# Optimization experiments

Measured on AMD Instinct MI355X. Metric: run time of the kernel, lower is better.

The kernel has to match this reference:

```python
import jax, jax.numpy as jnp
import numpy as np

B, T, N, F, H, HEADS = 4, 10, 2048, 64, 128, 4
D = H // HEADS
E = 65536
NTOT = B * N


def setup_inputs() -> dict:
    key = jax.random.key(0)
    ks = jax.random.split(key, 16)
    s = 0.05
    return {
        "x": jax.random.normal(ks[0], (B, T, N, F), jnp.float32),
        "W": jax.random.normal(ks[1], (F, H), jnp.float32) * s,
        "att_src": jax.random.normal(ks[2], (HEADS, D), jnp.float32) * s,
        "att_dst": jax.random.normal(ks[3], (HEADS, D), jnp.float32) * s,
        "gat_bias": jnp.zeros((H,), jnp.float32),
        "W_ih0": jax.random.normal(ks[4], (4 * H, H), jnp.float32) * s,
        "W_hh0": jax.random.normal(ks[5], (4 * H, H), jnp.float32) * s,
        "b_ih0": jnp.zeros((4 * H,), jnp.float32),
        "b_hh0": jnp.zeros((4 * H,), jnp.float32),
        "W_ih1": jax.random.normal(ks[6], (4 * H, H), jnp.float32) * s,
        "W_hh1": jax.random.normal(ks[7], (4 * H, H), jnp.float32) * s,
        "b_ih1": jnp.zeros((4 * H,), jnp.float32),
        "b_hh1": jnp.zeros((4 * H,), jnp.float32),
        "ln_gamma": jnp.ones((H,), jnp.float32),
        "ln_beta": jnp.zeros((H,), jnp.float32),
        "edge_index": jax.random.randint(ks[8], (2, E), 0, NTOT, dtype=jnp.int32),
    }


def reference(x, W, att_src, att_dst, gat_bias,
              W_ih0, W_hh0, b_ih0, b_hh0,
              W_ih1, W_hh1, b_ih1, b_hh1,
              ln_gamma, ln_beta, edge_index):
    # ---- GAT spatial encoding, vectorized over all T timesteps ----
    loops = jnp.arange(NTOT, dtype=edge_index.dtype)  # PyG GATConv adds self-loops
    src = jnp.concatenate([edge_index[0], loops])
    dst = jnp.concatenate([edge_index[1], loops])

    x_flat = x.transpose(1, 0, 2, 3).reshape(T, NTOT, F)          # [T, B*N, F]
    h = (x_flat @ W).reshape(T, NTOT, HEADS, D)                    # per-head projections
    a_src = jnp.einsum('tnhd,hd->tnh', h, att_src)                 # [T, NTOT, HEADS]
    a_dst = jnp.einsum('tnhd,hd->tnh', h, att_dst)
    e = jax.nn.leaky_relu(a_src[:, src] + a_dst[:, dst], 0.2)      # [T, Ef, HEADS]

    def seg_softmax(e_t):
        m = jax.ops.segment_max(e_t, dst, num_segments=NTOT)
        ex = jnp.exp(e_t - m[dst])
        den = jax.ops.segment_sum(ex, dst, num_segments=NTOT)
        return ex / den[dst]

    alpha = jax.vmap(seg_softmax)(e)                               # edge softmax per target
    msg = alpha[..., None] * h[:, src]                             # [T, Ef, HEADS, D]
    agg = jax.vmap(lambda m: jax.ops.segment_sum(m, dst, num_segments=NTOT))(msg)
    spatial = jax.nn.relu(agg.reshape(T, NTOT, H) + gat_bias)      # concat heads + bias + relu

    # ---- 2-layer LSTM over time (batched over all B*N node sequences) ----
    def step(carry, xt):
        h0, c0, h1, c1 = carry
        g0 = xt @ W_ih0.T + h0 @ W_hh0.T + (b_ih0 + b_hh0)
        i, f, g, o = jnp.split(g0, 4, axis=-1)
        c0 = jax.nn.sigmoid(f) * c0 + jax.nn.sigmoid(i) * jnp.tanh(g)
        h0 = jax.nn.sigmoid(o) * jnp.tanh(c0)
        g1 = h0 @ W_ih1.T + h1 @ W_hh1.T + (b_ih1 + b_hh1)
        i, f, g, o = jnp.split(g1, 4, axis=-1)
        c1 = jax.nn.sigmoid(f) * c1 + jax.nn.sigmoid(i) * jnp.tanh(g)
        h1 = jax.nn.sigmoid(o) * jnp.tanh(c1)
        return (h0, c0, h1, c1), None

    z = jnp.zeros((NTOT, H), spatial.dtype)
    (_, _, h1, _), _ = jax.lax.scan(step, (z, z, z, z), spatial)
    ctx = h1.reshape(B, N, H)

    # ---- LayerNorm ----
    mu = ctx.mean(-1, keepdims=True)
    var = ctx.var(-1, keepdims=True)
    return (ctx - mu) / jnp.sqrt(var + 1e-5) * ln_gamma + ln_beta
```

## Files before the change

### kernel.cpp

```cpp
#include <hip/hip_runtime.h>

#define T_ 10
#define B_ 4
#define N_ 2048
#define NTOT 8192
#define F_ 64
#define H_ 128
#define NHEADS 4
#define D_ 32
#define E_ 65536
#define EF 73728
#define HPAD 136

typedef __bf16 bf16x8 __attribute__((ext_vector_type(8)));
typedef float f32x4 __attribute__((ext_vector_type(4)));
typedef unsigned short u16;

__device__ __forceinline__ float bf2f(u16 u){
  union { unsigned int i; float f; } v; v.i = ((unsigned int)u) << 16; return v.f;
}
__device__ __forceinline__ u16 f2bf(float f){
  union { float f; unsigned int i; } v; v.f = f;
  return (u16)((v.i + 0x7FFFu + ((v.i >> 16) & 1u)) >> 16);
}
__device__ __forceinline__ float rcpf(float x){ return __builtin_amdgcn_rcpf(x); }
__device__ __forceinline__ float sigf(float x){ return rcpf(1.f + __expf(-x)); }
__device__ __forceinline__ float tanhfast(float x){ return 1.f - 2.f * rcpf(__expf(2.f * x) + 1.f); }
__device__ __forceinline__ float lrelu(float x){ return x > 0.f ? x : 0.2f * x; }

__global__ __launch_bounds__(256) void k_init(int* __restrict__ cnt){
  int i = blockIdx.x * 256 + threadIdx.x;
  if(i < NTOT) cnt[i] = 0;
}

__global__ __launch_bounds__(256) void k_count(const int* __restrict__ ei, int* __restrict__ cnt){
  int e = blockIdx.x * 256 + threadIdx.x;
  if(e < E_) atomicAdd(&cnt[ei[E_ + e]], 1);
}

__global__ __launch_bounds__(1024) void k_scan(const int* __restrict__ cnt,
                                               int* __restrict__ rowst,
                                               int* __restrict__ cursor){
  __shared__ int lds[1024];
  const int t = threadIdx.x;
  int loc[8];
  int s = 0;
  #pragma unroll
  for(int i = 0; i < 8; i++){ loc[i] = s; s += cnt[t * 8 + i]; }
  lds[t] = s;
  __syncthreads();
  for(int off = 1; off < 1024; off <<= 1){
    int v = lds[t];
    int a = (t >= off) ? lds[t - off] : 0;
    __syncthreads();
    lds[t] = v + a;
    __syncthreads();
  }
  const int base = (t > 0) ? lds[t - 1] : 0;
  #pragma unroll
  for(int i = 0; i < 8; i++){
    rowst[t * 8 + i] = base + loc[i];
    cursor[t * 8 + i] = 0;
  }
  if(t == 1023) rowst[NTOT] = lds[1023];
}

__global__ __launch_bounds__(256) void k_fill(const int* __restrict__ ei,
                                              const int* __restrict__ rowst,
                                              int* __restrict__ cursor,
                                              int* __restrict__ csr,
                                              int* __restrict__ csr_dst){
  int e = blockIdx.x * 256 + threadIdx.x;
  if(e < E_){
    int d = ei[E_ + e];
    int pos = atomicAdd(&cursor[d], 1);
    csr[rowst[d] + pos] = ei[e];
    csr_dst[rowst[d] + pos] = d;
  }
}

__global__ __launch_bounds__(256) void k_wconv(const float* __restrict__ s0, u16* __restrict__ d0,
                                               const float* __restrict__ s1, u16* __restrict__ d1,
                                               const float* __restrict__ s2, u16* __restrict__ d2,
                                               const float* __restrict__ s3, u16* __restrict__ d3,
                                               const float* __restrict__ W, u16* __restrict__ Wt){
  int i = blockIdx.x * 256 + threadIdx.x;
  if(blockIdx.y == 4){
    if(i < H_ * F_){
      int nn = i >> 6, f = i & 63;
      Wt[i] = f2bf(W[f * H_ + nn]);
    }
    return;
  }
  const float* src = blockIdx.y == 0 ? s0 : blockIdx.y == 1 ? s1 : blockIdx.y == 2 ? s2 : s3;
  u16* dst = blockIdx.y == 0 ? d0 : blockIdx.y == 1 ? d1 : blockIdx.y == 2 ? d2 : d3;
  if(i < 512 * 128){
    int p = i >> 7, k = i & 127;
    int w = p >> 6, g = (p >> 4) & 3, l = p & 15;
    int row = g * 128 + w * 16 + l;
    dst[i] = f2bf(src[row * 128 + k]);
  }
}

__global__ __launch_bounds__(256) void k_projm(const float* __restrict__ x,
    const u16* __restrict__ Wt, const float* __restrict__ att_s, const float* __restrict__ att_d,
    u16* __restrict__ hbuf, float* __restrict__ asrc, float* __restrict__ adst){
  const int tid  = threadIdx.x;
  const int wave = tid >> 6;
  const int lane = tid & 63;
  const int l15  = lane & 15;
  const int quad = lane >> 4;
  const int r0   = blockIdx.x * 64 + wave * 16;
  const int row  = r0 + l15;
  const int t = row >> 13, nt = row & 8191;
  const int b = nt >> 11, n = nt & 2047;
  const float* xrow = x + (((size_t)b * T_ + t) * N_ + n) * F_;

  bf16x8 a[2];
  #pragma unroll
  for(int ks = 0; ks < 2; ks++){
    const float4 f0 = *(const float4*)(xrow + ks * 32 + quad * 8);
    const float4 f1 = *(const float4*)(xrow + ks * 32 + quad * 8 + 4);
    bf16x8 av;
    av[0] = (__bf16)f0.x; av[1] = (__bf16)f0.y; av[2] = (__bf16)f0.z; av[3] = (__bf16)f0.w;
    av[4] = (__bf16)f1.x; av[5] = (__bf16)f1.y; av[6] = (__bf16)f1.z; av[7] = (__bf16)f1.w;
    a[ks] = av;
  }

  f32x4 acc[8];
  #pragma unroll
  for(int c = 0; c < 8; c++){ f32x4 z = {0.f,0.f,0.f,0.f}; acc[c] = z; }
  #pragma unroll
  for(int c = 0; c < 8; c++){
    #pragma unroll
    for(int ks = 0; ks < 2; ks++){
      const bf16x8 bv = *(const bf16x8*)(Wt + (c * 16 + l15) * F_ + ks * 32 + quad * 8);
      acc[c] = __builtin_amdgcn_mfma_f32_16x16x32_bf16(a[ks], bv, acc[c], 0, 0, 0);
    }
  }

  float ps[4][4], pd[4][4];
  #pragma unroll
  for(int r = 0; r < 4; r++)
    #pragma unroll
    for(int h = 0; h < 4; h++){ ps[r][h] = 0.f; pd[r][h] = 0.f; }

  #pragma unroll
  for(int c = 0; c < 8; c++){
    const int col = c * 16 + l15;
    const float asv = att_s[col];
    const float adv = att_d[col];
    const int head = c >> 1;
    #pragma unroll
    for(int r = 0; r < 4; r++){
      const float v = acc[c][r];
      hbuf[(size_t)(r0 + quad * 4 + r) * H_ + col] = f2bf(v);
      ps[r][head] += v * asv;
      pd[r][head] += v * adv;
    }
  }
  #pragma unroll
  for(int m = 8; m >= 1; m >>= 1){
    #pragma unroll
    for(int r = 0; r < 4; r++)
      #pragma unroll
      for(int h = 0; h < 4; h++){
        ps[r][h] += __shfl_xor(ps[r][h], m);
        pd[r][h] += __shfl_xor(pd[r][h], m);
      }
  }
  if(l15 == 0){
    #pragma unroll
    for(int r = 0; r < 4; r++){
      const int rw = r0 + quad * 4 + r;
      #pragma unroll
      for(int h = 0; h < 4; h++){
        asrc[(size_t)rw * NHEADS + h] = ps[r][h];
        adst[(size_t)rw * NHEADS + h] = pd[r][h];
      }
    }
  }
}

__global__ __launch_bounds__(256) void k_gat(const u16* __restrict__ hbuf,
    const float* __restrict__ asrc, const float* __restrict__ adst,
    const int* __restrict__ rowst, const int* __restrict__ csr,
    const float* __restrict__ gbias, u16* __restrict__ spat){
  __shared__ float exl[4][64][4];
  __shared__ int   sxl[4][64];
  const int tid = threadIdx.x;
  const int wave = tid >> 6;
  const int lane = tid & 63;
  const int task = blockIdx.x * 4 + wave;
  const int node = task & 8191;
  const int t = task >> 13;
  const int rbase = t * NTOT;
  const int rs = rowst[node], re = rowst[node + 1];

  const float4 ad4  = *(const float4*)&adst[(size_t)(rbase + node) * NHEADS];
  const float4 ass4 = *(const float4*)&asrc[(size_t)(rbase + node) * NHEADS];
  const float es0 = lrelu(ass4.x + ad4.x), es1 = lrelu(ass4.y + ad4.y);
  const float es2 = lrelu(ass4.z + ad4.z), es3 = lrelu(ass4.w + ad4.w);

  float m0 = es0, m1 = es1, m2 = es2, m3 = es3;
  float fe0 = 0.f, fe1 = 0.f, fe2 = 0.f, fe3 = 0.f;
  int   fs  = -1;
  {
    int i = rs + lane;
    if(i < re){
      fs = csr[i];
      const float4 as4 = *(const float4*)&asrc[(size_t)(rbase + fs) * NHEADS];
      fe0 = lrelu(as4.x + ad4.x); fe1 = lrelu(as4.y + ad4.y);
      fe2 = lrelu(as4.z + ad4.z); fe3 = lrelu(as4.w + ad4.w);
      m0 = fmaxf(m0, fe0); m1 = fmaxf(m1, fe1);
      m2 = fmaxf(m2, fe2); m3 = fmaxf(m3, fe3);
      for(i += 64; i < re; i += 64){
        const int s = csr[i];
        const float4 a2 = *(const float4*)&asrc[(size_t)(rbase + s) * NHEADS];
        m0 = fmaxf(m0, lrelu(a2.x + ad4.x)); m1 = fmaxf(m1, lrelu(a2.y + ad4.y));
        m2 = fmaxf(m2, lrelu(a2.z + ad4.z)); m3 = fmaxf(m3, lrelu(a2.w + ad4.w));
      }
    }
  }
  #pragma unroll
  for(int msk = 32; msk >= 1; msk >>= 1){
    m0 = fmaxf(m0, __shfl_xor(m0, msk));
    m1 = fmaxf(m1, __shfl_xor(m1, msk));
    m2 = fmaxf(m2, __shfl_xor(m2, msk));
    m3 = fmaxf(m3, __shfl_xor(m3, msk));
  }

  const int dlo = lane, dhi = lane + 64;
  float den0 = 0.f, den1 = 0.f, den2 = 0.f, den3 = 0.f;
  float accR0 = 0.f, accR1 = 0.f;
  for(int base = rs; base < re; base += 64){
    const int i = base + lane;
    float ex0 = 0.f, ex1 = 0.f, ex2 = 0.f, ex3 = 0.f;
    int sv = 0;
    if(i < re){
      float e0, e1, e2, e3;
      if(base == rs){ e0 = fe0; e1 = fe1; e2 = fe2; e3 = fe3; sv = fs; }
      else {
        sv = csr[i];
        const float4 a2 = *(const float4*)&asrc[(size_t)(rbase + sv) * NHEADS];
        e0 = lrelu(a2.x + ad4.x); e1 = lrelu(a2.y + ad4.y);
        e2 = lrelu(a2.z + ad4.z); e3 = lrelu(a2.w + ad4.w);
      }
      ex0 = __expf(e0 - m0); ex1 = __expf(e1 - m1);
      ex2 = __expf(e2 - m2); ex3 = __expf(e3 - m3);
      den0 += ex0; den1 += ex1; den2 += ex2; den3 += ex3;
    }
    exl[wave][lane][0] = ex0; exl[wave][lane][1] = ex1;
    exl[wave][lane][2] = ex2; exl[wave][lane][3] = ex3;
    sxl[wave][lane] = sv;
    __asm__ volatile("s_waitcnt lgkmcnt(0)" ::: "memory");
    __builtin_amdgcn_sched_barrier(0);
    const int lim = (re - base < 64) ? (re - base) : 64;
    for(int j = 0; j < lim; j++){
      const int s = sxl[wave][j];
      const float exA = lane < 32 ? exl[wave][j][0] : exl[wave][j][1];
      const float exB = lane < 32 ? exl[wave][j][2] : exl[wave][j][3];
      accR0 += exA * bf2f(hbuf[(size_t)(rbase + s) * H_ + dlo]);
      accR1 += exB * bf2f(hbuf[(size_t)(rbase + s) * H_ + dhi]);
    }
  }
  #pragma unroll
  for(int msk = 32; msk >= 1; msk >>= 1){
    den0 += __shfl_xor(den0, msk); den1 += __shfl_xor(den1, msk);
    den2 += __shfl_xor(den2, msk); den3 += __shfl_xor(den3, msk);
  }
  const float xs0 = __expf(es0 - m0), xs1 = __expf(es1 - m1);
  const float xs2 = __expf(es2 - m2), xs3 = __expf(es3 - m3);
  den0 += xs0; den1 += xs1; den2 += xs2; den3 += xs3;

  const float rdA = rcpf(lane < 32 ? den0 : den1);
  const float rdB = rcpf(lane < 32 ? den2 : den3);
  const float xsA = lane < 32 ? xs0 : xs1;
  const float xsB = lane < 32 ? xs2 : xs3;
  accR0 += xsA * bf2f(hbuf[(size_t)(rbase + node) * H_ + dlo]);
  accR1 += xsB * bf2f(hbuf[(size_t)(rbase + node) * H_ + dhi]);
  const float v0 = accR0 * rdA + gbias[dlo];
  const float v1 = accR1 * rdB + gbias[dhi];
  spat[(size_t)(rbase + node) * H_ + dlo] = f2bf(v0 > 0.f ? v0 : 0.f);
  spat[(size_t)(rbase + node) * H_ + dhi] = f2bf(v1 > 0.f ? v1 : 0.f);
}

__global__ __launch_bounds__(512) void k_lstm(
    const u16* __restrict__ spat,
    const u16* __restrict__ Wp_ih0, const u16* __restrict__ Wp_hh0,
    const float* __restrict__ bih0, const float* __restrict__ bhh0,
    const u16* __restrict__ Wp_ih1, const u16* __restrict__ Wp_hh1,
    const float* __restrict__ bih1, const float* __restrict__ bhh1,
    const float* __restrict__ lng, const float* __restrict__ lnb,
    float* __restrict__ out)
{
  __shared__ __align__(16) u16 xin[32 * HPAD];
  __shared__ __align__(16) u16 h0s[2][32 * HPAD];
  __shared__ __align__(16) u16 h1s[2][32 * HPAD];
  __shared__ __align__(16) float hfin[32 * 129];
  __shared__ float cst_l[16][512];
  __shared__ float bias_l[8][512];

  const int tid  = threadIdx.x;
  const int wave = tid >> 6;
  const int lane = tid & 63;
  const int l15  = lane & 15;
  const int quad = lane >> 4;
  const int n0   = blockIdx.x * 32;
  const int dim  = wave * 16 + l15;

  for(int i = tid; i < 2 * 32 * HPAD; i += 512){
    ((u16*)h0s)[i] = 0; ((u16*)h1s)[i] = 0;
  }
  {
    const u16* src = spat + (size_t)n0 * H_;
    const int r = tid >> 4, c = tid & 15;
    *(uint4*)(xin + r * HPAD + c * 8) = *(const uint4*)(src + r * 128 + c * 8);
  }
  #pragma unroll
  for(int i = 0; i < 16; i++) cst_l[i][tid] = 0.f;
  #pragma unroll
  for(int g = 0; g < 4; g++){
    bias_l[g][tid]     = bih0[g * 128 + dim] + bhh0[g * 128 + dim];
    bias_l[4 + g][tid] = bih1[g * 128 + dim] + bhh1[g * 128 + dim];
  }
  __syncthreads();

  const size_t fbase = (size_t)(wave * 64 + l15) * 128 + quad * 8;

#define LOADB(BK, MATB, KS, NTO)                                          \
    BK[0] = *(const bf16x8*)((MATB) + (NTO) * 2048 + (KS) * 32);          \
    BK[1] = *(const bf16x8*)((MATB) + ((NTO) + 1) * 2048 + (KS) * 32);

#define LOADA(AP, KS)                                                     \
    a0 = *(const bf16x8*)((AP) + l15 * HPAD + (KS) * 32 + quad * 8);      \
    a1 = *(const bf16x8*)((AP) + (16 + l15) * HPAD + (KS) * 32 + quad * 8);

#define MM(BK, NTO)                                                                             \
    acc[0][NTO]       = __builtin_amdgcn_mfma_f32_16x16x32_bf16(a0, BK[0], acc[0][NTO], 0, 0, 0);       \
    acc[1][NTO]       = __builtin_amdgcn_mfma_f32_16x16x32_bf16(a1, BK[0], acc[1][NTO], 0, 0, 0);       \
    acc[0][(NTO) + 1] = __builtin_amdgcn_mfma_f32_16x16x32_bf16(a0, BK[1], acc[0][(NTO) + 1], 0, 0, 0); \
    acc[1][(NTO) + 1] = __builtin_amdgcn_mfma_f32_16x16x32_bf16(a1, BK[1], acc[1][(NTO) + 1], 0, 0, 0); \
    __builtin_amdgcn_sched_barrier(0);

  #pragma unroll 1
  for(int t = 0; t < T_; t++){
    const int rp = t & 1, wp = rp ^ 1;
    #pragma unroll
    for(int layer = 0; layer < 2; layer++){
      const u16* Wih = layer ? Wp_ih1 : Wp_ih0;
      const u16* Whh = layer ? Wp_hh1 : Wp_hh0;
      const u16* xp  = layer ? h0s[wp] : xin;
      const u16* hp  = layer ? h1s[rp] : h0s[rp];

      f32x4 acc[2][4];
      #pragma unroll
      for(int nt = 0; nt < 4; nt++){
        const float bv = bias_l[layer * 4 + nt][tid];
        f32x4 b4 = {bv, bv, bv, bv};
        acc[0][nt] = b4; acc[1][nt] = b4;
      }

      const u16* WihB = Wih + fbase;
      const u16* WhhB = Whh + fbase;
      bf16x8 bA[2], bB[2], bC[2];
      bf16x8 a0, a1;

      LOADB(bA, WihB, 0, 0)  LOADB(bB, WihB, 0, 2)  LOADA(xp, 0)
      LOADB(bC, WihB, 1, 0)  MM(bA, 0)
      LOADB(bA, WihB, 1, 2)  MM(bB, 2)
      LOADA(xp, 1)  LOADB(bB, WihB, 2, 0)  MM(bC, 0)
      LOADB(bC, WihB, 2, 2)  MM(bA, 2)
      LOADA(xp, 2)  LOADB(bA, WihB, 3, 0)  MM(bB, 0)
      LOADB(bB, WihB, 3, 2)  MM(bC, 2)
      LOADA(xp, 3)  LOADB(bC, WhhB, 0, 0)  MM(bA, 0)
      LOADB(bA, WhhB, 0, 2)  MM(bB, 2)
      LOADA(hp, 0)  LOADB(bB, WhhB, 1, 0)  MM(bC, 0)
      LOADB(bC, WhhB, 1, 2)  MM(bA, 2)
      LOADA(hp, 1)  LOADB(bA, WhhB, 2, 0)  MM(bB, 0)
      LOADB(bB, WhhB, 2, 2)  MM(bC, 2)
      LOADA(hp, 2)  LOADB(bC, WhhB, 3, 0)  MM(bA, 0)
      LOADB(bA, WhhB, 3, 2)  MM(bB, 2)
      LOADA(hp, 3)  MM(bC, 0)
      MM(bA, 2)

      u16* hcur = layer ? h1s[wp] : h0s[wp];
      #pragma unroll
      for(int mt = 0; mt < 2; mt++){
        #pragma unroll
        for(int r = 0; r < 4; r++){
          const int node = mt * 16 + quad * 4 + r;
          const float gi = acc[mt][0][r];
          const float gf = acc[mt][1][r];
          const float gg = acc[mt][2][r];
          const float go = acc[mt][3][r];
          const int ci = layer * 8 + mt * 4 + r;
          const float c = sigf(gf) * cst_l[ci][tid] + sigf(gi) * tanhfast(gg);
          cst_l[ci][tid] = c;
          const float hv = sigf(go) * tanhfast(c);
          hcur[node * HPAD + dim] = f2bf(hv);
          if(layer == 1 && t == T_ - 1)
            hfin[node * 129 + dim] = hv;
        }
      }
      if(layer == 1 && t < T_ - 1){
        const u16* src = spat + (size_t)((t + 1) * NTOT + n0) * H_;
        const int r = tid >> 4, c = tid & 15;
        *(uint4*)(xin + r * HPAD + c * 8) = *(const uint4*)(src + r * 128 + c * 8);
      }
      __syncthreads();
    }
  }
#undef MM
#undef LOADA
#undef LOADB

  {
    const int node = tid >> 4;
    const int c0 = (tid & 15) * 8;
    float v[8];
    #pragma unroll
    for(int j = 0; j < 8; j++) v[j] = hfin[node * 129 + c0 + j];
    float s = 0.f;
    #pragma unroll
    for(int j = 0; j < 8; j++) s += v[j];
    #pragma unroll
    for(int m = 8; m >= 1; m >>= 1) s += __shfl_xor(s, m);
    const float mu = s * (1.f / H_);
    float q = 0.f;
    #pragma unroll
    for(int j = 0; j < 8; j++){ const float d = v[j] - mu; q += d * d; }
    #pragma unroll
    for(int m = 8; m >= 1; m >>= 1) q += __shfl_xor(q, m);
    const float rstd = rsqrtf(q * (1.f / H_) + 1e-5f);
    #pragma unroll
    for(int j = 0; j < 8; j++)
      out[(size_t)(n0 + node) * H_ + c0 + j] = (v[j] - mu) * rstd * lng[c0 + j] + lnb[c0 + j];
  }
}

extern "C" void kernel_launch(void* const* d_in, const int* in_sizes, int n_in,
                              void* d_out, int out_size, void* d_ws, size_t ws_size,
                              hipStream_t stream) {
  (void)in_sizes; (void)n_in; (void)out_size; (void)ws_size;
  const float* x     = (const float*)d_in[0];
  const float* W     = (const float*)d_in[1];
  const float* att_s = (const float*)d_in[2];
  const float* att_d = (const float*)d_in[3];
  const float* gbias = (const float*)d_in[4];
  const float* Wih0  = (const float*)d_in[5];
  const float* Whh0  = (const float*)d_in[6];
  const float* bih0  = (const float*)d_in[7];
  const float* bhh0  = (const float*)d_in[8];
  const float* Wih1  = (const float*)d_in[9];
  const float* Whh1  = (const float*)d_in[10];
  const float* bih1  = (const float*)d_in[11];
  const float* bhh1  = (const float*)d_in[12];
  const float* lng   = (const float*)d_in[13];
  const float* lnb   = (const float*)d_in[14];
  const int*   ei    = (const int*)d_in[15];
  float* out = (float*)d_out;

  char* p = (char*)d_ws;
  auto carve = [&](size_t bytes) -> void* {
    void* r = (void*)p;
    p += (bytes + 255) & ~(size_t)255;
    return r;
  };
  u16* Wp_ih0 = (u16*)carve(512 * 128 * 2);
  u16* Wp_hh0 = (u16*)carve(512 * 128 * 2);
  u16* Wp_ih1 = (u16*)carve(512 * 128 * 2);
  u16* Wp_hh1 = (u16*)carve(512 * 128 * 2);
  u16* Wt     = (u16*)carve(H_ * F_ * 2);
  u16*   hbuf   = (u16*)carve((size_t)T_ * NTOT * H_ * 2);
  float* asrc   = (float*)carve((size_t)T_ * NTOT * NHEADS * 4);
  float* adst   = (float*)carve((size_t)T_ * NTOT * NHEADS * 4);
  u16*   spat   = (u16*)carve((size_t)T_ * NTOT * H_ * 2);
  int*   cnt    = (int*)carve(NTOT * 4);
  int*   curs   = (int*)carve(NTOT * 4);
  int*   rowst  = (int*)carve((NTOT + 1) * 4);
  int*   csr    = (int*)carve((size_t)E_ * 4);
  int*   csrd   = (int*)carve((size_t)E_ * 4);

  hipLaunchKernelGGL(k_init,  dim3(32),        dim3(256),  0, stream, cnt);
  hipLaunchKernelGGL(k_count, dim3(256),       dim3(256),  0, stream, ei, cnt);
  hipLaunchKernelGGL(k_scan,  dim3(1),         dim3(1024), 0, stream, cnt, rowst, curs);
  hipLaunchKernelGGL(k_fill,  dim3(256),       dim3(256),  0, stream, ei, rowst, curs, csr, csrd);
  hipLaunchKernelGGL(k_wconv, dim3(256, 5),    dim3(256),  0, stream,
                     Wih0, Wp_ih0, Whh0, Wp_hh0, Wih1, Wp_ih1, Whh1, Wp_hh1, W, Wt);
  hipLaunchKernelGGL(k_projm, dim3(1280),      dim3(256),  0, stream, x, Wt, att_s, att_d, hbuf, asrc, adst);
  hipLaunchKernelGGL(k_gat,   dim3(20480),     dim3(256),  0, stream, hbuf, asrc, adst, rowst, csr, gbias, spat);
  hipLaunchKernelGGL(k_lstm,  dim3(256),       dim3(512),  0, stream, spat,
                     Wp_ih0, Wp_hh0, bih0, bhh0, Wp_ih1, Wp_hh1, bih1, bhh1, lng, lnb, out);
}
```

Baseline: 315.3 us.

## Stage LSTM weights through per-wave LDS double buffer, keep cell state in registers

Replaces the direct global-to-register weight fragment loads in the LSTM kernel with a software pipeline that prefetches weight slices into registers and stages them through a per-wave double-buffered LDS region ahead of the MFMAs. Cell state and biases move from shared memory into registers, and the kernel adds a waves-per-EU hint. The aim is to hide global load latency behind matrix ops and cut LDS traffic for state. The cost is extra LDS writes and reads per k-step, higher register pressure, and reliance on intra-wave ordering without explicit barriers on the per-wave buffer.

```diff
diff --git a/kernel.cpp b/kernel.cpp
--- a/kernel.cpp
+++ b/kernel.cpp
@@ -285,7 +285,7 @@
   spat[(size_t)(rbase + node) * H_ + dhi] = f2bf(v1 > 0.f ? v1 : 0.f);
 }
 
-__global__ __launch_bounds__(512) void k_lstm(
+__global__ __launch_bounds__(512) __attribute__((amdgpu_waves_per_eu(2))) void k_lstm(
     const u16* __restrict__ spat,
     const u16* __restrict__ Wp_ih0, const u16* __restrict__ Wp_hh0,
     const float* __restrict__ bih0, const float* __restrict__ bhh0,
@@ -294,12 +294,11 @@
     const float* __restrict__ lng, const float* __restrict__ lnb,
     float* __restrict__ out)
 {
+  __shared__ __align__(16) unsigned char wbuf[8][2][4096];
   __shared__ __align__(16) u16 xin[32 * HPAD];
   __shared__ __align__(16) u16 h0s[2][32 * HPAD];
   __shared__ __align__(16) u16 h1s[2][32 * HPAD];
   __shared__ __align__(16) float hfin[32 * 129];
-  __shared__ float cst_l[16][512];
-  __shared__ float bias_l[8][512];
 
   const int tid  = threadIdx.x;
   const int wave = tid >> 6;
@@ -317,31 +316,21 @@
     const int r = tid >> 4, c = tid & 15;
     *(uint4*)(xin + r * HPAD + c * 8) = *(const uint4*)(src + r * 128 + c * 8);
   }
-  #pragma unroll
-  for(int i = 0; i < 16; i++) cst_l[i][tid] = 0.f;
+  float cst[16];
+  #pragma unroll
+  for(int i = 0; i < 16; i++) cst[i] = 0.f;
+
+  float bias[2][4];
   #pragma unroll
   for(int g = 0; g < 4; g++){
-    bias_l[g][tid]     = bih0[g * 128 + dim] + bhh0[g * 128 + dim];
-    bias_l[4 + g][tid] = bih1[g * 128 + dim] + bhh1[g * 128 + dim];
+    bias[0][g] = bih0[g * 128 + dim] + bhh0[g * 128 + dim];
+    bias[1][g] = bih1[g * 128 + dim] + bhh1[g * 128 + dim];
   }
   __syncthreads();
 
-  const size_t fbase = (size_t)(wave * 64 + l15) * 128 + quad * 8;
-
-#define LOADB(BK, MATB, KS, NTO)                                          \
-    BK[0] = *(const bf16x8*)((MATB) + (NTO) * 2048 + (KS) * 32);          \
-    BK[1] = *(const bf16x8*)((MATB) + ((NTO) + 1) * 2048 + (KS) * 32);
-
-#define LOADA(AP, KS)                                                     \
-    a0 = *(const bf16x8*)((AP) + l15 * HPAD + (KS) * 32 + quad * 8);      \
-    a1 = *(const bf16x8*)((AP) + (16 + l15) * HPAD + (KS) * 32 + quad * 8);
-
-#define MM(BK, NTO)                                                                             \
-    acc[0][NTO]       = __builtin_amdgcn_mfma_f32_16x16x32_bf16(a0, BK[0], acc[0][NTO], 0, 0, 0);       \
-    acc[1][NTO]       = __builtin_amdgcn_mfma_f32_16x16x32_bf16(a1, BK[0], acc[1][NTO], 0, 0, 0);       \
-    acc[0][(NTO) + 1] = __builtin_amdgcn_mfma_f32_16x16x32_bf16(a0, BK[1], acc[0][(NTO) + 1], 0, 0, 0); \
-    acc[1][(NTO) + 1] = __builtin_amdgcn_mfma_f32_16x16x32_bf16(a1, BK[1], acc[1][(NTO) + 1], 0, 0, 0); \
-    __builtin_amdgcn_sched_barrier(0);
+  unsigned char* wbuf_w = &wbuf[wave][0][0];
+  const size_t loff = (size_t)(wave * 64 + l15) * 128 + quad * 8;
+  uint4 sA0, sB0, sC0, sD0, sA1, sB1, sC1, sD1;
 
   #pragma unroll 1
   for(int t = 0; t < T_; t++){
@@ -356,33 +345,77 @@
       f32x4 acc[2][4];
       #pragma unroll
       for(int nt = 0; nt < 4; nt++){
-        const float bv = bias_l[layer * 4 + nt][tid];
+        const float bv = bias[layer][nt];
         f32x4 b4 = {bv, bv, bv, bv};
         acc[0][nt] = b4; acc[1][nt] = b4;
       }
 
-      const u16* WihB = Wih + fbase;
-      const u16* WhhB = Whh + fbase;
-      bf16x8 bA[2], bB[2], bC[2];
-      bf16x8 a0, a1;
-
-      LOADB(bA, WihB, 0, 0)  LOADB(bB, WihB, 0, 2)  LOADA(xp, 0)
-      LOADB(bC, WihB, 1, 0)  MM(bA, 0)
-      LOADB(bA, WihB, 1, 2)  MM(bB, 2)
-      LOADA(xp, 1)  LOADB(bB, WihB, 2, 0)  MM(bC, 0)
-      LOADB(bC, WihB, 2, 2)  MM(bA, 2)
-      LOADA(xp, 2)  LOADB(bA, WihB, 3, 0)  MM(bB, 0)
-      LOADB(bB, WihB, 3, 2)  MM(bC, 2)
-      LOADA(xp, 3)  LOADB(bC, WhhB, 0, 0)  MM(bA, 0)
-      LOADB(bA, WhhB, 0, 2)  MM(bB, 2)
-      LOADA(hp, 0)  LOADB(bB, WhhB, 1, 0)  MM(bC, 0)
-      LOADB(bC, WhhB, 1, 2)  MM(bA, 2)
-      LOADA(hp, 1)  LOADB(bA, WhhB, 2, 0)  MM(bB, 0)
-      LOADB(bB, WhhB, 2, 2)  MM(bC, 2)
-      LOADA(hp, 2)  LOADB(bC, WhhB, 3, 0)  MM(bA, 0)
-      LOADB(bA, WhhB, 3, 2)  MM(bB, 2)
-      LOADA(hp, 3)  MM(bC, 0)
-      MM(bA, 2)
+      {
+        const u16* g0 = Wih + loff;
+        sA0 = *(const uint4*)(g0);        sB0 = *(const uint4*)(g0 + 2048);
+        sC0 = *(const uint4*)(g0 + 4096); sD0 = *(const uint4*)(g0 + 6144);
+        unsigned char* wd = wbuf_w + lane * 16;
+        *(uint4*)(wd) = sA0;        *(uint4*)(wd + 1024) = sB0;
+        *(uint4*)(wd + 2048) = sC0; *(uint4*)(wd + 3072) = sD0;
+        const u16* g1 = Wih + loff + 32;
+        sA1 = *(const uint4*)(g1);        sB1 = *(const uint4*)(g1 + 2048);
+        sC1 = *(const uint4*)(g1 + 4096); sD1 = *(const uint4*)(g1 + 6144);
+        const u16* g2 = Wih + loff + 64;
+        sA0 = *(const uint4*)(g2);        sB0 = *(const uint4*)(g2 + 2048);
+        sC0 = *(const uint4*)(g2 + 4096); sD0 = *(const uint4*)(g2 + 6144);
+      }
+
+      #pragma unroll 1
+      for(int pp = 0; pp < 4; pp++){
+        const int p0 = pp * 2;
+        {
+          unsigned char* wd = wbuf_w + 4096 + lane * 16;
+          *(uint4*)(wd) = sA1;        *(uint4*)(wd + 1024) = sB1;
+          *(uint4*)(wd + 2048) = sC1; *(uint4*)(wd + 3072) = sD1;
+          if(p0 < 5){
+            const int q = p0 + 3;
+            const u16* g = ((q < 4) ? Wih : Whh) + loff + (q & 3) * 32;
+            sA1 = *(const uint4*)(g);        sB1 = *(const uint4*)(g + 2048);
+            sC1 = *(const uint4*)(g + 4096); sD1 = *(const uint4*)(g + 6144);
+          }
+          const u16* ap = (p0 < 4) ? xp : hp;
+          const int ka = (p0 & 3) * 32 + quad * 8;
+          const bf16x8 a0 = *(const bf16x8*)(ap + l15 * HPAD + ka);
+          const bf16x8 a1 = *(const bf16x8*)(ap + (16 + l15) * HPAD + ka);
+          const unsigned char* rb = wbuf_w;
+          #pragma unroll
+          for(int nt = 0; nt < 4; nt++){
+            const bf16x8 b = *(const bf16x8*)(rb + nt * 1024 + lane * 16);
+            acc[0][nt] = __builtin_amdgcn_mfma_f32_16x16x32_bf16(a0, b, acc[0][nt], 0, 0, 0);
+            acc[1][nt] = __builtin_amdgcn_mfma_f32_16x16x32_bf16(a1, b, acc[1][nt], 0, 0, 0);
+          }
+        }
+        const int p1 = p0 + 1;
+        {
+          if(p1 < 7){
+            unsigned char* wd = wbuf_w + lane * 16;
+            *(uint4*)(wd) = sA0;        *(uint4*)(wd + 1024) = sB0;
+            *(uint4*)(wd + 2048) = sC0; *(uint4*)(wd + 3072) = sD0;
+          }
+          if(p1 < 5){
+            const int q = p1 + 3;
+            const u16* g = Whh + loff + (q & 3) * 32;
+            sA0 = *(const uint4*)(g);        sB0 = *(const uint4*)(g + 2048);
+            sC0 = *(const uint4*)(g + 4096); sD0 = *(const uint4*)(g + 6144);
+          }
+          const u16* ap = (p1 < 4) ? xp : hp;
+          const int ka = (p1 & 3) * 32 + quad * 8;
+          const bf16x8 a0 = *(const bf16x8*)(ap + l15 * HPAD + ka);
+          const bf16x8 a1 = *(const bf16x8*)(ap + (16 + l15) * HPAD + ka);
+          const unsigned char* rb = wbuf_w + 4096;
+          #pragma unroll
+          for(int nt = 0; nt < 4; nt++){
+            const bf16x8 b = *(const bf16x8*)(rb + nt * 1024 + lane * 16);
+            acc[0][nt] = __builtin_amdgcn_mfma_f32_16x16x32_bf16(a0, b, acc[0][nt], 0, 0, 0);
+            acc[1][nt] = __builtin_amdgcn_mfma_f32_16x16x32_bf16(a1, b, acc[1][nt], 0, 0, 0);
+          }
+        }
+      }
 
       u16* hcur = layer ? h1s[wp] : h0s[wp];
       #pragma unroll
@@ -395,8 +428,8 @@
           const float gg = acc[mt][2][r];
           const float go = acc[mt][3][r];
           const int ci = layer * 8 + mt * 4 + r;
-          const float c = sigf(gf) * cst_l[ci][tid] + sigf(gi) * tanhfast(gg);
-          cst_l[ci][tid] = c;
+          const float c = sigf(gf) * cst[ci] + sigf(gi) * tanhfast(gg);
+          cst[ci] = c;
           const float hv = sigf(go) * tanhfast(c);
           hcur[node * HPAD + dim] = f2bf(hv);
           if(layer == 1 && t == T_ - 1)
@@ -411,9 +444,6 @@
       __syncthreads();
     }
   }
-#undef MM
-#undef LOADA
-#undef LOADB
 
   {
     const int node = tid >> 4;
```

Result: no change. 318.1 us (+0.9%).
